# Kernel tuning notes

Hardware: AMD Instinct MI355X
Metric: run time of the kernel (lower is better)

Reference implementation:

```python
import jax, jax.numpy as jnp
import numpy as np

N = 12288
F_DIM = 512
H1 = 32
H2 = 16
E_RAND = N * 32  # 393216 random edges; self-loops appended (DGL graph built from adj + I)


def setup_inputs() -> dict:
    key = jax.random.key(0)
    ks = jax.random.split(key, 8)
    feat = jax.random.normal(ks[0], (N, F_DIM), dtype=jnp.float32)
    src_r = jax.random.randint(ks[1], (E_RAND,), 0, N, dtype=jnp.int32)
    dst_r = jax.random.randint(ks[2], (E_RAND,), 0, N, dtype=jnp.int32)
    loop = jnp.arange(N, dtype=jnp.int32)
    src = jnp.concatenate([src_r, loop])  # [E_RAND + N]
    dst = jnp.concatenate([dst_r, loop])
    s1 = 1.0 / np.sqrt(F_DIM)
    s2 = 1.0 / np.sqrt(H1)
    W1 = jax.random.normal(ks[3], (F_DIM, H1), dtype=jnp.float32) * s1
    W2 = jax.random.normal(ks[4], (H1, H2), dtype=jnp.float32) * s2
    W3 = jax.random.normal(ks[5], (H1, H2), dtype=jnp.float32) * s2
    b1 = jnp.zeros((H1,), jnp.float32)
    b2 = jnp.zeros((H2,), jnp.float32)
    b3 = jnp.zeros((H2,), jnp.float32)
    return {"feat": feat, "src": src, "dst": dst,
            "W1": W1, "b1": b1, "W2": W2, "b2": b2, "W3": W3, "b3": b3}


def _norms(src, dst):
    ones = jnp.ones(src.shape[0], jnp.float32)
    deg_out = jax.ops.segment_sum(ones, src, num_segments=N)
    deg_in = jax.ops.segment_sum(ones, dst, num_segments=N)
    inv_sqrt_out = jnp.where(deg_out > 0, jax.lax.rsqrt(jnp.maximum(deg_out, 1.0)), 0.0)
    inv_sqrt_in = jnp.where(deg_in > 0, jax.lax.rsqrt(jnp.maximum(deg_in, 1.0)), 0.0)
    return inv_sqrt_out, inv_sqrt_in


def _graph_conv(x, src, dst, n_src, n_dst, W, b):
    # DGL GraphConv, norm='both': D_in^{-1/2} * A_agg( D_out^{-1/2} * x ) @ W + b
    # (project first when in_dim > out_dim is math-equivalent; do agg-then-W here)
    xn = x * n_src[:, None]
    msg = xn[src]  # gather along edges  [E, d]
    agg = jax.ops.segment_sum(msg, dst, num_segments=N)  # scatter-add SpMM
    h = agg * n_dst[:, None]
    return h @ W + b


def reference(feat, src, dst, W1, b1, W2, b2, W3, b3):
    n_src, n_dst = _norms(src, dst)
    h1 = jax.nn.relu(_graph_conv(feat, src, dst, n_src, n_dst, W1, b1))
    mu = _graph_conv(h1, src, dst, n_src, n_dst, W2, b2)
    logvar = _graph_conv(h1, src, dst, n_src, n_dst, W3, b3)
    # eval-mode reparameterize -> z = mu; InnerProductDecoder with identity act
    z = mu
    adj_rec = z @ z.T  # [N, N] logits
    return adj_rec, mu, logvar
```

## Files before the change

### kernel.cpp

```cpp
#include <hip/hip_runtime.h>
#include <cstddef>

#define NN 12288
#define FD 512
#define H1 32
#define H2 16
#define CAP 80
#define GEMM_BLOCKS 192

typedef float floatx4 __attribute__((ext_vector_type(4)));
typedef float floatx2 __attribute__((ext_vector_type(2)));

__global__ __launch_bounds__(256) void k_fused1(const float* __restrict__ feat,
                                                const float* __restrict__ W1,
                                                float* __restrict__ P,
                                                const int* __restrict__ src,
                                                const int* __restrict__ dst,
                                                int* __restrict__ cnt,
                                                int* __restrict__ deg_out,
                                                int* __restrict__ bucket, int E) {
    if (blockIdx.x < GEMM_BLOCKS) {
        __shared__ float Wlds[FD * H1];
        int tid = threadIdx.x;
        for (int t = tid; t < FD * H1 / 4; t += 256) {
            ((float4*)Wlds)[t] = ((const float4*)W1)[t];
        }
        __syncthreads();

        int row = blockIdx.x * 64 + (tid >> 2);
        int cg  = (tid & 3) * 8;
        float acc[8] = {};
        const float4* f4 = (const float4*)(feat + (size_t)row * FD);
#pragma unroll 4
        for (int k4 = 0; k4 < FD / 4; ++k4) {
            float4 f = f4[k4];
            const float* w = &Wlds[(k4 * 4) * H1 + cg];
#pragma unroll
            for (int j = 0; j < 8; ++j) {
                acc[j] += f.x * w[j] + f.y * w[H1 + j] + f.z * w[2 * H1 + j] + f.w * w[3 * H1 + j];
            }
        }
#pragma unroll
        for (int j = 0; j < 8; ++j) P[(size_t)row * H1 + cg + j] = acc[j];
    } else {
        int t = (blockIdx.x - GEMM_BLOCKS) * 256 + threadIdx.x;
        int E4 = E >> 2;
        if (t < E4) {
            int4 s = ((const int4*)src)[t];
            int4 d = ((const int4*)dst)[t];
            atomicAdd(&deg_out[s.x], 1); atomicAdd(&deg_out[s.y], 1);
            atomicAdd(&deg_out[s.z], 1); atomicAdd(&deg_out[s.w], 1);
            int sl;
            sl = atomicAdd(&cnt[d.x], 1); if (sl < CAP) bucket[d.x * CAP + sl] = s.x;
            sl = atomicAdd(&cnt[d.y], 1); if (sl < CAP) bucket[d.y * CAP + sl] = s.y;
            sl = atomicAdd(&cnt[d.z], 1); if (sl < CAP) bucket[d.z * CAP + sl] = s.z;
            sl = atomicAdd(&cnt[d.w], 1); if (sl < CAP) bucket[d.w * CAP + sl] = s.w;
        }
        if (t == 0) {
            for (int e = E4 * 4; e < E; ++e) {
                atomicAdd(&deg_out[src[e]], 1);
                int d = dst[e];
                int sl = atomicAdd(&cnt[d], 1);
                if (sl < CAP) bucket[d * CAP + sl] = src[e];
            }
        }
    }
}

__global__ __launch_bounds__(256) void k_agg1(const int* __restrict__ cnt,
                                              const int* __restrict__ deg_out,
                                              const int* __restrict__ bucket,
                                              const float* __restrict__ P,
                                              const float* __restrict__ b1,
                                              float* __restrict__ h1s) {
    int r = blockIdx.x * 8 + (threadIdx.x >> 5);
    int j = threadIdx.x & 31;
    int deg = cnt[r];
    const int* bk = bucket + (size_t)r * CAP;
    float sA = 0.0f, sB = 0.0f;
    int e = 0;
    for (; e + 3 < deg; e += 4) {
        int s0 = bk[e], s1 = bk[e + 1], s2 = bk[e + 2], s3 = bk[e + 3];
        float w0 = rsqrtf((float)deg_out[s0]), w1 = rsqrtf((float)deg_out[s1]);
        float w2 = rsqrtf((float)deg_out[s2]), w3 = rsqrtf((float)deg_out[s3]);
        sA += w0 * P[(size_t)s0 * H1 + j] + w1 * P[(size_t)s1 * H1 + j];
        sB += w2 * P[(size_t)s2 * H1 + j] + w3 * P[(size_t)s3 * H1 + j];
    }
    for (; e < deg; ++e) {
        int s0 = bk[e];
        sA += rsqrtf((float)deg_out[s0]) * P[(size_t)s0 * H1 + j];
    }
    float ndst = rsqrtf((float)deg);
    float nsr  = rsqrtf((float)deg_out[r]);
    float h = fmaxf((sA + sB) * ndst + b1[j], 0.0f);
    h1s[(size_t)r * H1 + j] = h * nsr;
}

__global__ __launch_bounds__(256) void k_agg2(const int* __restrict__ cnt,
                                              const int* __restrict__ bucket,
                                              const float* __restrict__ h1s,
                                              const float* __restrict__ W2, const float* __restrict__ b2,
                                              const float* __restrict__ W3, const float* __restrict__ b3,
                                              float* __restrict__ mu, float* __restrict__ lv) {
    __shared__ float W2l[H1 * H2], W3l[H1 * H2];
    __shared__ float S[8][H1];
    int tid = threadIdx.x;
    for (int t = tid; t < H1 * H2; t += 256) { W2l[t] = W2[t]; W3l[t] = W3[t]; }

    int r0 = blockIdx.x * 8;
    int rl = tid >> 5, j = tid & 31;
    int r = r0 + rl;
    int deg = cnt[r];
    const int* bk = bucket + (size_t)r * CAP;
    float sA = 0.0f, sB = 0.0f;
    int e = 0;
    for (; e + 3 < deg; e += 4) {
        int s0 = bk[e], s1 = bk[e + 1], s2 = bk[e + 2], s3 = bk[e + 3];
        sA += h1s[(size_t)s0 * H1 + j] + h1s[(size_t)s1 * H1 + j];
        sB += h1s[(size_t)s2 * H1 + j] + h1s[(size_t)s3 * H1 + j];
    }
    for (; e < deg; ++e) sA += h1s[(size_t)bk[e] * H1 + j];
    S[rl][j] = (sA + sB) * rsqrtf((float)deg);
    __syncthreads();

    int rr = tid >> 5;
    int c = tid & 15;
    bool is_lv = (tid & 16) != 0;
    const float* W = is_lv ? W3l : W2l;
    float acc = is_lv ? b3[c] : b2[c];
#pragma unroll
    for (int k = 0; k < H1; ++k) acc += S[rr][k] * W[k * H2 + c];
    float* o = is_lv ? lv : mu;
    o[(size_t)(r0 + rr) * H2 + c] = acc;
}

#define TI 128
#define TJ 256
__global__ __launch_bounds__(256, 2) void k_adj(const float* __restrict__ mu, float* __restrict__ out) {
    __shared__ float Alt[H2][TI];
    __shared__ float Blt[H2][TJ];
    int tid = threadIdx.x;
    int i0 = blockIdx.y * TI;
    int j0 = blockIdx.x * TJ;

    {
        int row = tid >> 1;
        int h8  = (tid & 1) * 8;
        float4 a0 = *(const float4*)&mu[(size_t)(i0 + row) * H2 + h8];
        float4 a1 = *(const float4*)&mu[(size_t)(i0 + row) * H2 + h8 + 4];
        Alt[h8 + 0][row] = a0.x; Alt[h8 + 1][row] = a0.y; Alt[h8 + 2][row] = a0.z; Alt[h8 + 3][row] = a0.w;
        Alt[h8 + 4][row] = a1.x; Alt[h8 + 5][row] = a1.y; Alt[h8 + 6][row] = a1.z; Alt[h8 + 7][row] = a1.w;
        float4 b0 = *(const float4*)&mu[(size_t)(j0 + tid) * H2 + 0];
        float4 b1 = *(const float4*)&mu[(size_t)(j0 + tid) * H2 + 4];
        float4 b2 = *(const float4*)&mu[(size_t)(j0 + tid) * H2 + 8];
        float4 b3 = *(const float4*)&mu[(size_t)(j0 + tid) * H2 + 12];
        Blt[0][tid] = b0.x; Blt[1][tid] = b0.y; Blt[2][tid] = b0.z; Blt[3][tid] = b0.w;
        Blt[4][tid] = b1.x; Blt[5][tid] = b1.y; Blt[6][tid] = b1.z; Blt[7][tid] = b1.w;
        Blt[8][tid] = b2.x; Blt[9][tid] = b2.y; Blt[10][tid] = b2.z; Blt[11][tid] = b2.w;
        Blt[12][tid] = b3.x; Blt[13][tid] = b3.y; Blt[14][tid] = b3.z; Blt[15][tid] = b3.w;
    }
    __syncthreads();

    int tx = tid & 15;
    int ty = tid >> 4;
    floatx2 acc2[8][8] = {};
#pragma unroll 2
    for (int k = 0; k < H2; ++k) {
        floatx4 a0 = *(const floatx4*)&Alt[k][ty * 8];
        floatx4 a1 = *(const floatx4*)&Alt[k][ty * 8 + 4];
        float a[8] = {a0.x, a0.y, a0.z, a0.w, a1.x, a1.y, a1.z, a1.w};
        floatx2 bp[8];
#pragma unroll
        for (int g = 0; g < 4; ++g) {
            floatx4 b = *(const floatx4*)&Blt[k][g * 64 + tx * 4];
            bp[2 * g]     = (floatx2){b.x, b.y};
            bp[2 * g + 1] = (floatx2){b.z, b.w};
        }
#pragma unroll
        for (int ii = 0; ii < 8; ++ii) {
            floatx2 av = (floatx2){a[ii], a[ii]};
#pragma unroll
            for (int jp = 0; jp < 8; ++jp)
                acc2[ii][jp] = __builtin_elementwise_fma(av, bp[jp], acc2[ii][jp]);
        }
    }

#pragma unroll
    for (int ii = 0; ii < 8; ++ii) {
        size_t row = (size_t)(i0 + ty * 8 + ii);
#pragma unroll
        for (int g = 0; g < 4; ++g) {
            float4 v = make_float4(acc2[ii][2 * g].x, acc2[ii][2 * g].y,
                                   acc2[ii][2 * g + 1].x, acc2[ii][2 * g + 1].y);
            *(float4*)&out[row * NN + j0 + g * 64 + tx * 4] = v;
        }
    }
}

extern "C" void kernel_launch(void* const* d_in, const int* in_sizes, int n_in,
                              void* d_out, int out_size, void* d_ws, size_t ws_size,
                              hipStream_t stream) {
    const float* feat = (const float*)d_in[0];
    const int*   src  = (const int*)d_in[1];
    const int*   dst  = (const int*)d_in[2];
    const float* W1   = (const float*)d_in[3];
    const float* b1   = (const float*)d_in[4];
    const float* W2   = (const float*)d_in[5];
    const float* b2   = (const float*)d_in[6];
    const float* W3   = (const float*)d_in[7];
    const float* b3   = (const float*)d_in[8];
    int E = in_sizes[1];

    int* iws = (int*)d_ws;
    int* cnt     = iws;
    int* deg_out = iws + NN;
    int* bucket  = iws + 2 * NN;
    float* fws = (float*)(iws + 2 * NN + NN * CAP);
    float* P   = fws;
    float* h1s = fws + NN * H1;

    float* adj = (float*)d_out;
    float* mu  = adj + (size_t)NN * NN;
    float* lv  = mu + (size_t)NN * H2;

    hipMemsetAsync(iws, 0, 2 * NN * sizeof(int), stream);

    int eb4 = ((E >> 2) + 255) / 256;
    k_fused1<<<GEMM_BLOCKS + eb4, 256, 0, stream>>>(feat, W1, P, src, dst,
                                                    cnt, deg_out, bucket, E);
    k_agg1<<<NN / 8, 256, 0, stream>>>(cnt, deg_out, bucket, P, b1, h1s);
    k_agg2<<<NN / 8, 256, 0, stream>>>(cnt, bucket, h1s, W2, b2, W3, b3, mu, lv);

    dim3 grid(NN / TJ, NN / TI);
    k_adj<<<grid, 256, 0, stream>>>(mu, adj);
}
```

Before: 219.3 us.

## Fuse all GCN stages into one persistent cooperative kernel with grid syncs

Replaces the memset and four separate kernel launches with a single cooperative persistent kernel that zeroes counters, runs the feature GEMM and edge bucketing, both aggregations, and the z·zT tile GEMM, separated by grid-wide syncs. The goal is to remove launch gaps and the tail effects between stages. In exchange it adds grid.sync cost and caps the grid at 4 blocks per CU. It also reads W1 from global memory instead of LDS and shrinks the adj tiles to 64 rows. The old multi-kernel path remains only as a fallback if the cooperative launch fails.

```diff
diff --git a/kernel.cpp b/kernel.cpp
--- a/kernel.cpp
+++ b/kernel.cpp
@@ -1,5 +1,8 @@
 #include <hip/hip_runtime.h>
+#include <hip/hip_cooperative_groups.h>
 #include <cstddef>
+
+namespace cg = cooperative_groups;
 
 #define NN 12288
 #define FD 512
@@ -8,8 +11,207 @@
 #define CAP 80
 #define GEMM_BLOCKS 192
 
+#define TI 64
+#define TJ 256
+#define NTI (NN / TI)
+#define NTJ (NN / TJ)
+#define NTILES (NTI * NTJ)
+
 typedef float floatx4 __attribute__((ext_vector_type(4)));
 typedef float floatx2 __attribute__((ext_vector_type(2)));
+
+__global__ __launch_bounds__(256, 4) void k_mega(
+    const float* __restrict__ feat, const float* __restrict__ W1,
+    const int* __restrict__ src, const int* __restrict__ dst,
+    const float* __restrict__ b1,
+    const float* __restrict__ W2, const float* __restrict__ b2,
+    const float* __restrict__ W3, const float* __restrict__ b3,
+    int* __restrict__ cnt, int* __restrict__ deg_out, int* __restrict__ bucket,
+    float* __restrict__ P, float* __restrict__ h1s,
+    float* __restrict__ mu, float* __restrict__ lv,
+    float* __restrict__ adj, int E)
+{
+    cg::grid_group grid = cg::this_grid();
+    __shared__ float LDS[5120];
+    const int tid = threadIdx.x;
+    const int nb = gridDim.x;
+
+    for (int i = blockIdx.x * 256 + tid; i < 2 * NN; i += nb * 256) cnt[i] = 0;
+    grid.sync();
+
+    {
+        const int lane = tid & 63;
+        const int wv   = tid >> 6;
+        const int j    = lane & 31;
+        const int sub  = lane >> 5;
+        for (int rb = blockIdx.x; rb < NN / 32; rb += nb) {
+            int r0 = rb * 32 + wv * 8 + sub * 4;
+            float a0 = 0, a1 = 0, a2 = 0, a3 = 0;
+            const float4* f0 = (const float4*)(feat + (size_t)r0 * FD);
+            const float4* f1 = (const float4*)(feat + (size_t)(r0 + 1) * FD);
+            const float4* f2 = (const float4*)(feat + (size_t)(r0 + 2) * FD);
+            const float4* f3 = (const float4*)(feat + (size_t)(r0 + 3) * FD);
+#pragma unroll 4
+            for (int k4 = 0; k4 < FD / 4; ++k4) {
+                float4 fa = f0[k4], fb = f1[k4], fc = f2[k4], fd = f3[k4];
+                float w0 = W1[(k4 * 4 + 0) * H1 + j];
+                float w1 = W1[(k4 * 4 + 1) * H1 + j];
+                float w2 = W1[(k4 * 4 + 2) * H1 + j];
+                float w3 = W1[(k4 * 4 + 3) * H1 + j];
+                a0 += fa.x * w0 + fa.y * w1 + fa.z * w2 + fa.w * w3;
+                a1 += fb.x * w0 + fb.y * w1 + fb.z * w2 + fb.w * w3;
+                a2 += fc.x * w0 + fc.y * w1 + fc.z * w2 + fc.w * w3;
+                a3 += fd.x * w0 + fd.y * w1 + fd.z * w2 + fd.w * w3;
+            }
+            P[(size_t)r0 * H1 + j]       = a0;
+            P[(size_t)(r0 + 1) * H1 + j] = a1;
+            P[(size_t)(r0 + 2) * H1 + j] = a2;
+            P[(size_t)(r0 + 3) * H1 + j] = a3;
+        }
+        int E4 = E >> 2;
+        for (int t = blockIdx.x * 256 + tid; t < E4; t += nb * 256) {
+            int4 s = ((const int4*)src)[t];
+            int4 d = ((const int4*)dst)[t];
+            atomicAdd(&deg_out[s.x], 1); atomicAdd(&deg_out[s.y], 1);
+            atomicAdd(&deg_out[s.z], 1); atomicAdd(&deg_out[s.w], 1);
+            int sl;
+            sl = atomicAdd(&cnt[d.x], 1); if (sl < CAP) bucket[d.x * CAP + sl] = s.x;
+            sl = atomicAdd(&cnt[d.y], 1); if (sl < CAP) bucket[d.y * CAP + sl] = s.y;
+            sl = atomicAdd(&cnt[d.z], 1); if (sl < CAP) bucket[d.z * CAP + sl] = s.z;
+            sl = atomicAdd(&cnt[d.w], 1); if (sl < CAP) bucket[d.w * CAP + sl] = s.w;
+        }
+        if (blockIdx.x == 0 && tid == 0) {
+            for (int e = (E >> 2) << 2; e < E; ++e) {
+                atomicAdd(&deg_out[src[e]], 1);
+                int d = dst[e];
+                int sl = atomicAdd(&cnt[d], 1);
+                if (sl < CAP) bucket[d * CAP + sl] = src[e];
+            }
+        }
+    }
+    grid.sync();
+
+    {
+        const int rl = tid >> 5, j = tid & 31;
+        for (int g = blockIdx.x; g < NN / 8; g += nb) {
+            int r = g * 8 + rl;
+            int deg = cnt[r];
+            const int* bk = bucket + (size_t)r * CAP;
+            float sA = 0.0f, sB = 0.0f;
+            int e = 0;
+            for (; e + 3 < deg; e += 4) {
+                int s0 = bk[e], s1 = bk[e + 1], s2 = bk[e + 2], s3 = bk[e + 3];
+                float w0 = rsqrtf((float)deg_out[s0]), w1 = rsqrtf((float)deg_out[s1]);
+                float w2 = rsqrtf((float)deg_out[s2]), w3 = rsqrtf((float)deg_out[s3]);
+                sA += w0 * P[(size_t)s0 * H1 + j] + w1 * P[(size_t)s1 * H1 + j];
+                sB += w2 * P[(size_t)s2 * H1 + j] + w3 * P[(size_t)s3 * H1 + j];
+            }
+            for (; e < deg; ++e) {
+                int s0 = bk[e];
+                sA += rsqrtf((float)deg_out[s0]) * P[(size_t)s0 * H1 + j];
+            }
+            float h = fmaxf((sA + sB) * rsqrtf((float)deg) + b1[j], 0.0f);
+            h1s[(size_t)r * H1 + j] = h * rsqrtf((float)deg_out[r]);
+        }
+    }
+    grid.sync();
+
+    {
+        float* W2l = LDS;
+        float* W3l = LDS + 512;
+        float* S   = LDS + 1024;
+        for (int t = tid; t < H1 * H2; t += 256) { W2l[t] = W2[t]; W3l[t] = W3[t]; }
+        const int rl = tid >> 5, j = tid & 31;
+        const int rr = tid >> 5, c = tid & 15;
+        const bool is_lv = (tid & 16) != 0;
+        for (int g = blockIdx.x; g < NN / 8; g += nb) {
+            int r = g * 8 + rl;
+            int deg = cnt[r];
+            const int* bk = bucket + (size_t)r * CAP;
+            float sA = 0.0f, sB = 0.0f;
+            int e = 0;
+            for (; e + 3 < deg; e += 4) {
+                int s0 = bk[e], s1 = bk[e + 1], s2 = bk[e + 2], s3 = bk[e + 3];
+                sA += h1s[(size_t)s0 * H1 + j] + h1s[(size_t)s1 * H1 + j];
+                sB += h1s[(size_t)s2 * H1 + j] + h1s[(size_t)s3 * H1 + j];
+            }
+            for (; e < deg; ++e) sA += h1s[(size_t)bk[e] * H1 + j];
+            __syncthreads();
+            S[rl * H1 + j] = (sA + sB) * rsqrtf((float)deg);
+            __syncthreads();
+            const float* W = is_lv ? W3l : W2l;
+            float acc = is_lv ? b3[c] : b2[c];
+#pragma unroll
+            for (int k = 0; k < H1; ++k) acc += S[rr * H1 + k] * W[k * H2 + c];
+            float* o = is_lv ? lv : mu;
+            o[(size_t)(g * 8 + rr) * H2 + c] = acc;
+        }
+    }
+    grid.sync();
+
+    {
+        float* Alt = LDS;
+        float* Blt = LDS + TI * H2;
+        const int tx = tid & 15, ty = tid >> 4;
+        for (int tile = blockIdx.x; tile < NTILES; tile += nb) {
+            int i0 = (tile % NTI) * TI;
+            int j0 = (tile / NTI) * TJ;
+            __syncthreads();
+            {
+                int row = tid >> 2, seg = tid & 3;
+                float4 a = *(const float4*)&mu[(size_t)(i0 + row) * H2 + seg * 4];
+                Alt[(seg * 4 + 0) * TI + row] = a.x;
+                Alt[(seg * 4 + 1) * TI + row] = a.y;
+                Alt[(seg * 4 + 2) * TI + row] = a.z;
+                Alt[(seg * 4 + 3) * TI + row] = a.w;
+                float4 b0 = *(const float4*)&mu[(size_t)(j0 + tid) * H2 + 0];
+                float4 b1 = *(const float4*)&mu[(size_t)(j0 + tid) * H2 + 4];
+                float4 b2 = *(const float4*)&mu[(size_t)(j0 + tid) * H2 + 8];
+                float4 b3 = *(const float4*)&mu[(size_t)(j0 + tid) * H2 + 12];
+                Blt[0 * TJ + tid] = b0.x;  Blt[1 * TJ + tid] = b0.y;
+                Blt[2 * TJ + tid] = b0.z;  Blt[3 * TJ + tid] = b0.w;
+                Blt[4 * TJ + tid] = b1.x;  Blt[5 * TJ + tid] = b1.y;
+                Blt[6 * TJ + tid] = b1.z;  Blt[7 * TJ + tid] = b1.w;
+                Blt[8 * TJ + tid] = b2.x;  Blt[9 * TJ + tid] = b2.y;
+                Blt[10 * TJ + tid] = b2.z; Blt[11 * TJ + tid] = b2.w;
+                Blt[12 * TJ + tid] = b3.x; Blt[13 * TJ + tid] = b3.y;
+                Blt[14 * TJ + tid] = b3.z; Blt[15 * TJ + tid] = b3.w;
+            }
+            __syncthreads();
+
+            floatx2 acc2[4][8] = {};
+#pragma unroll 2
+            for (int k = 0; k < H2; ++k) {
+                floatx4 av4 = *(const floatx4*)&Alt[k * TI + ty * 4];
+                float a[4] = {av4.x, av4.y, av4.z, av4.w};
+                floatx2 bp[8];
+#pragma unroll
+                for (int g = 0; g < 4; ++g) {
+                    floatx4 b = *(const floatx4*)&Blt[k * TJ + g * 64 + tx * 4];
+                    bp[2 * g]     = (floatx2){b.x, b.y};
+                    bp[2 * g + 1] = (floatx2){b.z, b.w};
+                }
+#pragma unroll
+                for (int ii = 0; ii < 4; ++ii) {
+                    floatx2 avv = (floatx2){a[ii], a[ii]};
+#pragma unroll
+                    for (int jp = 0; jp < 8; ++jp)
+                        acc2[ii][jp] = __builtin_elementwise_fma(avv, bp[jp], acc2[ii][jp]);
+                }
+            }
+#pragma unroll
+            for (int ii = 0; ii < 4; ++ii) {
+                size_t row = (size_t)(i0 + ty * 4 + ii);
+#pragma unroll
+                for (int g = 0; g < 4; ++g) {
+                    float4 v = make_float4(acc2[ii][2 * g].x, acc2[ii][2 * g].y,
+                                           acc2[ii][2 * g + 1].x, acc2[ii][2 * g + 1].y);
+                    *(float4*)&adj[row * NN + j0 + g * 64 + tx * 4] = v;
+                }
+            }
+        }
+    }
+}
 
 __global__ __launch_bounds__(256) void k_fused1(const float* __restrict__ feat,
                                                 const float* __restrict__ W1,
@@ -22,11 +224,8 @@
     if (blockIdx.x < GEMM_BLOCKS) {
         __shared__ float Wlds[FD * H1];
         int tid = threadIdx.x;
-        for (int t = tid; t < FD * H1 / 4; t += 256) {
-            ((float4*)Wlds)[t] = ((const float4*)W1)[t];
-        }
+        for (int t = tid; t < FD * H1 / 4; t += 256) ((float4*)Wlds)[t] = ((const float4*)W1)[t];
         __syncthreads();
-
         int row = blockIdx.x * 64 + (tid >> 2);
         int cg  = (tid & 3) * 8;
         float acc[8] = {};
@@ -36,9 +235,8 @@
             float4 f = f4[k4];
             const float* w = &Wlds[(k4 * 4) * H1 + cg];
 #pragma unroll
-            for (int j = 0; j < 8; ++j) {
+            for (int j = 0; j < 8; ++j)
                 acc[j] += f.x * w[j] + f.y * w[H1 + j] + f.z * w[2 * H1 + j] + f.w * w[3 * H1 + j];
-            }
         }
 #pragma unroll
         for (int j = 0; j < 8; ++j) P[(size_t)row * H1 + cg + j] = acc[j];
@@ -86,14 +284,9 @@
         sA += w0 * P[(size_t)s0 * H1 + j] + w1 * P[(size_t)s1 * H1 + j];
         sB += w2 * P[(size_t)s2 * H1 + j] + w3 * P[(size_t)s3 * H1 + j];
     }
-    for (; e < deg; ++e) {
-        int s0 = bk[e];
-        sA += rsqrtf((float)deg_out[s0]) * P[(size_t)s0 * H1 + j];
-    }
-    float ndst = rsqrtf((float)deg);
-    float nsr  = rsqrtf((float)deg_out[r]);
-    float h = fmaxf((sA + sB) * ndst + b1[j], 0.0f);
-    h1s[(size_t)r * H1 + j] = h * nsr;
+    for (; e < deg; ++e) { int s0 = bk[e]; sA += rsqrtf((float)deg_out[s0]) * P[(size_t)s0 * H1 + j]; }
+    float h = fmaxf((sA + sB) * rsqrtf((float)deg) + b1[j], 0.0f);
+    h1s[(size_t)r * H1 + j] = h * rsqrtf((float)deg_out[r]);
 }
 
 __global__ __launch_bounds__(256) void k_agg2(const int* __restrict__ cnt,
@@ -106,7 +299,6 @@
     __shared__ float S[8][H1];
     int tid = threadIdx.x;
     for (int t = tid; t < H1 * H2; t += 256) { W2l[t] = W2[t]; W3l[t] = W3[t]; }
-
     int r0 = blockIdx.x * 8;
     int rl = tid >> 5, j = tid & 31;
     int r = r0 + rl;
@@ -122,9 +314,7 @@
     for (; e < deg; ++e) sA += h1s[(size_t)bk[e] * H1 + j];
     S[rl][j] = (sA + sB) * rsqrtf((float)deg);
     __syncthreads();
-
-    int rr = tid >> 5;
-    int c = tid & 15;
+    int rr = tid >> 5, c = tid & 15;
     bool is_lv = (tid & 16) != 0;
     const float* W = is_lv ? W3l : W2l;
     float acc = is_lv ? b3[c] : b2[c];
@@ -134,15 +324,14 @@
     o[(size_t)(r0 + rr) * H2 + c] = acc;
 }
 
-#define TI 128
-#define TJ 256
+#define FTI 128
+#define FTJ 256
 __global__ __launch_bounds__(256, 2) void k_adj(const float* __restrict__ mu, float* __restrict__ out) {
-    __shared__ float Alt[H2][TI];
-    __shared__ float Blt[H2][TJ];
+    __shared__ float Alt[H2][FTI];
+    __shared__ float Blt[H2][FTJ];
     int tid = threadIdx.x;
-    int i0 = blockIdx.y * TI;
-    int j0 = blockIdx.x * TJ;
-
+    int i0 = blockIdx.y * FTI;
+    int j0 = blockIdx.x * FTJ;
     {
         int row = tid >> 1;
         int h8  = (tid & 1) * 8;
@@ -160,7 +349,6 @@
         Blt[12][tid] = b3.x; Blt[13][tid] = b3.y; Blt[14][tid] = b3.z; Blt[15][tid] = b3.w;
     }
     __syncthreads();
-
     int tx = tid & 15;
     int ty = tid >> 4;
     floatx2 acc2[8][8] = {};
@@ -184,7 +372,6 @@
                 acc2[ii][jp] = __builtin_elementwise_fma(av, bp[jp], acc2[ii][jp]);
         }
     }
-
 #pragma unroll
     for (int ii = 0; ii < 8; ++ii) {
         size_t row = (size_t)(i0 + ty * 8 + ii);
@@ -223,14 +410,31 @@
     float* mu  = adj + (size_t)NN * NN;
     float* lv  = mu + (size_t)NN * H2;
 
-    hipMemsetAsync(iws, 0, 2 * NN * sizeof(int), stream);
-
-    int eb4 = ((E >> 2) + 255) / 256;
-    k_fused1<<<GEMM_BLOCKS + eb4, 256, 0, stream>>>(feat, W1, P, src, dst,
-                                                    cnt, deg_out, bucket, E);
-    k_agg1<<<NN / 8, 256, 0, stream>>>(cnt, deg_out, bucket, P, b1, h1s);
-    k_agg2<<<NN / 8, 256, 0, stream>>>(cnt, bucket, h1s, W2, b2, W3, b3, mu, lv);
-
-    dim3 grid(NN / TJ, NN / TI);
-    k_adj<<<grid, 256, 0, stream>>>(mu, adj);
-}
+    int dev = 0;
+    hipGetDevice(&dev);
+    int nCU = 0;
+    hipDeviceGetAttribute(&nCU, hipDeviceAttributeMultiprocessorCount, dev);
+    int bpc = 0;
+    hipOccupancyMaxActiveBlocksPerMultiprocessor(&bpc, k_mega, 256, 0);
+    if (nCU <= 0) nCU = 256;
+    if (bpc <= 0) bpc = 1;
+    if (bpc > 4) bpc = 4;
+    int nb = nCU * bpc;
+
+    void* args[] = { (void*)&feat, (void*)&W1, (void*)&src, (void*)&dst, (void*)&b1,
+                     (void*)&W2, (void*)&b2, (void*)&W3, (void*)&b3,
+                     (void*)&cnt, (void*)&deg_out, (void*)&bucket,
+                     (void*)&P, (void*)&h1s, (void*)&mu, (void*)&lv, (void*)&adj, (void*)&E };
+    hipError_t err = hipLaunchCooperativeKernel((void*)k_mega, dim3(nb), dim3(256),
+                                                args, 0, stream);
+    if (err != hipSuccess) {
+        hipMemsetAsync(iws, 0, 2 * NN * sizeof(int), stream);
+        int eb4 = ((E >> 2) + 255) / 256;
+        k_fused1<<<GEMM_BLOCKS + eb4, 256, 0, stream>>>(feat, W1, P, src, dst,
+                                                        cnt, deg_out, bucket, E);
+        k_agg1<<<NN / 8, 256, 0, stream>>>(cnt, deg_out, bucket, P, b1, h1s);
+        k_agg2<<<NN / 8, 256, 0, stream>>>(cnt, bucket, h1s, W2, b2, W3, b3, mu, lv);
+        dim3 grid(NN / FTJ, NN / FTI);
+        k_adj<<<grid, 256, 0, stream>>>(mu, adj);
+    }
+}
```

After: 464.1 us. 2.12x slower.

## Make adjacency blocks loop over column tiles with register-prefetched B tiles

Applied to the files above, without the earlier changes.

Each k_adj block now keeps its A tile resident and walks 12 consecutive 256-column tiles, prefetching the next B tile into registers while computing and storing the current one. The grid shrinks from 48x96 to 4x96 blocks, which amortizes A-tile loads and block launch overhead. The cost is fewer blocks (384) on a large GPU, which may underfill the CUs for this store-bound output, plus two extra barriers per tile. The agg1 change only inlines two temporaries.

```diff
diff --git a/kernel.cpp b/kernel.cpp
--- a/kernel.cpp
+++ b/kernel.cpp
@@ -90,10 +90,8 @@
         int s0 = bk[e];
         sA += rsqrtf((float)deg_out[s0]) * P[(size_t)s0 * H1 + j];
     }
-    float ndst = rsqrtf((float)deg);
-    float nsr  = rsqrtf((float)deg_out[r]);
-    float h = fmaxf((sA + sB) * ndst + b1[j], 0.0f);
-    h1s[(size_t)r * H1 + j] = h * nsr;
+    float h = fmaxf((sA + sB) * rsqrtf((float)deg) + b1[j], 0.0f);
+    h1s[(size_t)r * H1 + j] = h * rsqrtf((float)deg_out[r]);
 }
 
 __global__ __launch_bounds__(256) void k_agg2(const int* __restrict__ cnt,
@@ -136,12 +134,13 @@
 
 #define TI 128
 #define TJ 256
+#define CHUNK 12
 __global__ __launch_bounds__(256, 2) void k_adj(const float* __restrict__ mu, float* __restrict__ out) {
     __shared__ float Alt[H2][TI];
     __shared__ float Blt[H2][TJ];
     int tid = threadIdx.x;
     int i0 = blockIdx.y * TI;
-    int j0 = blockIdx.x * TJ;
+    int jbase = blockIdx.x * (TJ * CHUNK);
 
     {
         int row = tid >> 1;
@@ -150,49 +149,69 @@
         float4 a1 = *(const float4*)&mu[(size_t)(i0 + row) * H2 + h8 + 4];
         Alt[h8 + 0][row] = a0.x; Alt[h8 + 1][row] = a0.y; Alt[h8 + 2][row] = a0.z; Alt[h8 + 3][row] = a0.w;
         Alt[h8 + 4][row] = a1.x; Alt[h8 + 5][row] = a1.y; Alt[h8 + 6][row] = a1.z; Alt[h8 + 7][row] = a1.w;
-        float4 b0 = *(const float4*)&mu[(size_t)(j0 + tid) * H2 + 0];
-        float4 b1 = *(const float4*)&mu[(size_t)(j0 + tid) * H2 + 4];
-        float4 b2 = *(const float4*)&mu[(size_t)(j0 + tid) * H2 + 8];
-        float4 b3 = *(const float4*)&mu[(size_t)(j0 + tid) * H2 + 12];
-        Blt[0][tid] = b0.x; Blt[1][tid] = b0.y; Blt[2][tid] = b0.z; Blt[3][tid] = b0.w;
-        Blt[4][tid] = b1.x; Blt[5][tid] = b1.y; Blt[6][tid] = b1.z; Blt[7][tid] = b1.w;
-        Blt[8][tid] = b2.x; Blt[9][tid] = b2.y; Blt[10][tid] = b2.z; Blt[11][tid] = b2.w;
-        Blt[12][tid] = b3.x; Blt[13][tid] = b3.y; Blt[14][tid] = b3.z; Blt[15][tid] = b3.w;
+    }
+    float4 pb0, pb1, pb2, pb3;
+    {
+        const float* br = &mu[(size_t)(jbase + tid) * H2];
+        pb0 = *(const float4*)&br[0];  pb1 = *(const float4*)&br[4];
+        pb2 = *(const float4*)&br[8];  pb3 = *(const float4*)&br[12];
+        Blt[0][tid] = pb0.x;  Blt[1][tid] = pb0.y;  Blt[2][tid] = pb0.z;  Blt[3][tid] = pb0.w;
+        Blt[4][tid] = pb1.x;  Blt[5][tid] = pb1.y;  Blt[6][tid] = pb1.z;  Blt[7][tid] = pb1.w;
+        Blt[8][tid] = pb2.x;  Blt[9][tid] = pb2.y;  Blt[10][tid] = pb2.z; Blt[11][tid] = pb2.w;
+        Blt[12][tid] = pb3.x; Blt[13][tid] = pb3.y; Blt[14][tid] = pb3.z; Blt[15][tid] = pb3.w;
     }
     __syncthreads();
 
     int tx = tid & 15;
     int ty = tid >> 4;
-    floatx2 acc2[8][8] = {};
+    for (int t = 0; t < CHUNK; ++t) {
+        int j0 = jbase + t * TJ;
+        if (t + 1 < CHUNK) {
+            const float* br = &mu[(size_t)(j0 + TJ + tid) * H2];
+            pb0 = *(const float4*)&br[0];  pb1 = *(const float4*)&br[4];
+            pb2 = *(const float4*)&br[8];  pb3 = *(const float4*)&br[12];
+        }
+
+        floatx2 acc2[8][8] = {};
 #pragma unroll 2
-    for (int k = 0; k < H2; ++k) {
-        floatx4 a0 = *(const floatx4*)&Alt[k][ty * 8];
-        floatx4 a1 = *(const floatx4*)&Alt[k][ty * 8 + 4];
-        float a[8] = {a0.x, a0.y, a0.z, a0.w, a1.x, a1.y, a1.z, a1.w};
-        floatx2 bp[8];
-#pragma unroll
-        for (int g = 0; g < 4; ++g) {
-            floatx4 b = *(const floatx4*)&Blt[k][g * 64 + tx * 4];
-            bp[2 * g]     = (floatx2){b.x, b.y};
-            bp[2 * g + 1] = (floatx2){b.z, b.w};
-        }
+        for (int k = 0; k < H2; ++k) {
+            floatx4 a0 = *(const floatx4*)&Alt[k][ty * 8];
+            floatx4 a1 = *(const floatx4*)&Alt[k][ty * 8 + 4];
+            float a[8] = {a0.x, a0.y, a0.z, a0.w, a1.x, a1.y, a1.z, a1.w};
+            floatx2 bp[8];
+#pragma unroll
+            for (int g = 0; g < 4; ++g) {
+                floatx4 b = *(const floatx4*)&Blt[k][g * 64 + tx * 4];
+                bp[2 * g]     = (floatx2){b.x, b.y};
+                bp[2 * g + 1] = (floatx2){b.z, b.w};
+            }
+#pragma unroll
+            for (int ii = 0; ii < 8; ++ii) {
+                floatx2 av = (floatx2){a[ii], a[ii]};
+#pragma unroll
+                for (int jp = 0; jp < 8; ++jp)
+                    acc2[ii][jp] = __builtin_elementwise_fma(av, bp[jp], acc2[ii][jp]);
+            }
+        }
+
 #pragma unroll
         for (int ii = 0; ii < 8; ++ii) {
-            floatx2 av = (floatx2){a[ii], a[ii]};
-#pragma unroll
-            for (int jp = 0; jp < 8; ++jp)
-                acc2[ii][jp] = __builtin_elementwise_fma(av, bp[jp], acc2[ii][jp]);
-        }
-    }
-
-#pragma unroll
-    for (int ii = 0; ii < 8; ++ii) {
-        size_t row = (size_t)(i0 + ty * 8 + ii);
-#pragma unroll
-        for (int g = 0; g < 4; ++g) {
-            float4 v = make_float4(acc2[ii][2 * g].x, acc2[ii][2 * g].y,
-                                   acc2[ii][2 * g + 1].x, acc2[ii][2 * g + 1].y);
-            *(float4*)&out[row * NN + j0 + g * 64 + tx * 4] = v;
+            size_t row = (size_t)(i0 + ty * 8 + ii);
+#pragma unroll
+            for (int g = 0; g < 4; ++g) {
+                float4 v = make_float4(acc2[ii][2 * g].x, acc2[ii][2 * g].y,
+                                       acc2[ii][2 * g + 1].x, acc2[ii][2 * g + 1].y);
+                *(float4*)&out[row * NN + j0 + g * 64 + tx * 4] = v;
+            }
+        }
+
+        if (t + 1 < CHUNK) {
+            __syncthreads();
+            Blt[0][tid] = pb0.x;  Blt[1][tid] = pb0.y;  Blt[2][tid] = pb0.z;  Blt[3][tid] = pb0.w;
+            Blt[4][tid] = pb1.x;  Blt[5][tid] = pb1.y;  Blt[6][tid] = pb1.z;  Blt[7][tid] = pb1.w;
+            Blt[8][tid] = pb2.x;  Blt[9][tid] = pb2.y;  Blt[10][tid] = pb2.z; Blt[11][tid] = pb2.w;
+            Blt[12][tid] = pb3.x; Blt[13][tid] = pb3.y; Blt[14][tid] = pb3.z; Blt[15][tid] = pb3.w;
+            __syncthreads();
         }
     }
 }
@@ -231,6 +250,6 @@
     k_agg1<<<NN / 8, 256, 0, stream>>>(cnt, deg_out, bucket, P, b1, h1s);
     k_agg2<<<NN / 8, 256, 0, stream>>>(cnt, bucket, h1s, W2, b2, W3, b3, mu, lv);
 
-    dim3 grid(NN / TJ, NN / TI);
+    dim3 grid(NN / (TJ * CHUNK), NN / TI);
     k_adj<<<grid, 256, 0, stream>>>(mu, adj);
 }
```

Result: slower. 233.2 us (+6.3%).
